# Kernel tuning notes

Hardware: AMD Instinct MI355X
Metric: run time of the kernel (lower is better)

## Reference

```python
import jax, jax.numpy as jnp
import numpy as np

D_MODEL = 96
D_EXP = 192      # d_expand == d_inner (ssm_ratio=ssm_rank_ratio=2)
D_STATE = 16
DT_RANK = 6      # ceil(96/16)
DC_IN = 4        # dc_inner
DC_STATE = 16
DTC_RANK = 6
B, H, W = 2, 48, 48


def _ln_channel(x, w, b):
    # WithBias LayerNorm over channel dim (torch code reshapes b c h w -> b (hw) c)
    mu = x.mean(axis=1, keepdims=True)
    var = ((x - mu) ** 2).mean(axis=1, keepdims=True)
    return (x - mu) / jnp.sqrt(var + 1e-5) * w[None, :, None, None] + b[None, :, None, None]


def _selective_scan(u, delta, A, Bs, Cs, D, delta_bias):
    # u, delta: (b,k,d,l); A: (k,d,n); Bs,Cs: (b,k,n,l); D, delta_bias: (k,d)
    delta = jax.nn.softplus(delta + delta_bias[None, :, :, None])
    dA = jnp.exp(jnp.einsum('bkdl,kdn->bkldn', delta, A))          # decay per step
    dBu = jnp.einsum('bkdl,bkdl,bknl->bkldn', delta, u, Bs)        # input injection

    def combine(c1, c2):
        a1, b1 = c1
        a2, b2 = c2
        return a1 * a2, a2 * b1 + b2

    _, hs = jax.lax.associative_scan(combine, (dA, dBu), axis=2)   # parallel linear recurrence over l
    return jnp.einsum('bkldn,bknl->bkdl', hs, Cs) + D[None, :, :, None] * u


def _spatial_core(x, x_proj_w, dt_w, dt_b, A_logs, Ds, onw, onb):
    b, d, h, w = x.shape
    l = h * w
    # cross_scan_2d: row-major, col-major, and their flips -> (b,4,d,l)
    xs = jnp.stack([x.reshape(b, d, l), jnp.swapaxes(x, 2, 3).reshape(b, d, l)], 1)
    xs = jnp.concatenate([xs, jnp.flip(xs, -1)], 1)
    x_dbl = jnp.einsum('bkdl,kcd->bkcl', xs, x_proj_w)
    dts, Bs, Cs = jnp.split(x_dbl, [DT_RANK, DT_RANK + D_STATE], axis=2)
    dts = jnp.einsum('bkrl,kdr->bkdl', dts, dt_w)
    A = -jnp.exp(A_logs).reshape(4, d, D_STATE)
    out_y = _selective_scan(xs, dts, A, Bs, Cs, Ds.reshape(4, d), dt_b)  # (b,4,d,l)
    inv = jnp.flip(out_y[:, 2:4], -1)
    wh = jnp.swapaxes(out_y[:, 1].reshape(b, d, w, h), 2, 3).reshape(b, d, l)
    invwh = jnp.swapaxes(inv[:, 1].reshape(b, d, w, h), 2, 3).reshape(b, d, l)
    y = (out_y[:, 0] + inv[:, 0] + wh + invwh).reshape(b, d, h, w)
    return _ln_channel(y, onw, onb)


def _channel_core(y, cin_w, cin_b, cout_w, cout_b, xc_proj_w, dtc_w, dtc_b, Ac_logs, Dsc, cnw, cnb):
    b, d = y.shape[0], y.shape[1]
    xc = y.mean(axis=(2, 3))                                              # adaptive avg pool -> (b,d)
    xc = xc[:, None, :] * cin_w.reshape(1, DC_IN, 1) + cin_b.reshape(1, DC_IN, 1)  # 1x1 conv_cin -> (b,4,d)
    xsc = jnp.stack([xc, jnp.flip(xc, -1)], 1)                            # (b,2,dc,L=d)
    xc_dbl = jnp.einsum('bkdl,kcd->bkcl', xsc, xc_proj_w)
    dtsc, Bc, Cc = jnp.split(xc_dbl, [DTC_RANK, DTC_RANK + DC_STATE], axis=2)
    dtsc = jnp.einsum('bkrl,kdr->bkdl', dtsc, dtc_w)
    Ac = -jnp.exp(Ac_logs).reshape(2, DC_IN, DC_STATE)
    outc = _selective_scan(xsc, dtsc, Ac, Bc, Cc, Dsc.reshape(2, DC_IN), dtc_b)  # (b,2,dc,d)
    yc = outc[:, 0] + jnp.flip(outc[:, 1], -1)                            # merge fwd/bwd channel scans
    yc = jnp.einsum('bdl,d->bl', yc, cout_w.reshape(DC_IN)) + cout_b.reshape(())  # 1x1 conv_cout
    return _ln_channel(yc.reshape(b, d, 1, 1), cnw, cnb)


def _conv1x1(x, w, b):
    return jnp.einsum('bchw,oc->bohw', x, w.reshape(w.shape[0], w.shape[1])) + b[None, :, None, None]


def _forward(x, in_w, in_b, dw_w, dw_b, x_proj_w, dt_w, dt_b, A_logs, Ds, out_norm_w, out_norm_b,
             cin_w, cin_b, cout_w, cout_b, xc_proj_w, dtc_w, dtc_b, Ac_logs, Dsc, cn_w, cn_b,
             out_w, out_b):
    xz = _conv1x1(x, in_w, in_b)                      # (b, 2*d_expand, h, w)
    x1, z = xz[:, :D_EXP], xz[:, D_EXP:]
    z = jax.nn.silu(z)
    x1 = jax.lax.conv_general_dilated(x1, dw_w, (1, 1), 'SAME',
                                      dimension_numbers=('NCHW', 'OIHW', 'NCHW'),
                                      feature_group_count=D_EXP) + dw_b[None, :, None, None]
    x1 = jax.nn.silu(x1)
    y = _spatial_core(x1, x_proj_w, dt_w, dt_b, A_logs, Ds, out_norm_w, out_norm_b)
    c = _channel_core(y, cin_w, cin_b, cout_w, cout_b, xc_proj_w, dtc_w, dtc_b, Ac_logs, Dsc, cn_w, cn_b)
    y = y * c * z                                     # channel modulation + gating
    return _conv1x1(y, out_w, out_b)


def setup_inputs():
    key = jax.random.key(0)
    ks = jax.random.split(key, 24)
    s = 0.02

    def rn(k, shape, scale=s):
        return jax.random.normal(k, shape, jnp.float32) * scale

    A_logs = jnp.log(jnp.tile(jnp.arange(1, D_STATE + 1, dtype=jnp.float32)[None, :], (4 * D_EXP, 1)))
    return dict(
        x=jax.random.normal(ks[0], (B, D_MODEL, H, W), jnp.float32),
        in_w=rn(ks[1], (2 * D_EXP, D_MODEL, 1, 1)),
        in_b=rn(ks[2], (2 * D_EXP,)),
        dw_w=rn(ks[3], (D_EXP, 1, 3, 3)),
        dw_b=rn(ks[4], (D_EXP,)),
        x_proj_w=rn(ks[5], (4, DT_RANK + 2 * D_STATE, D_EXP)),
        dt_w=rn(ks[6], (4, D_EXP, DT_RANK), 0.1),
        dt_b=rn(ks[7], (4, D_EXP), 0.5) - 4.0,
        A_logs=A_logs,
        Ds=jnp.ones((4 * D_EXP,), jnp.float32),
        out_norm_w=jnp.ones((D_EXP,), jnp.float32),
        out_norm_b=jnp.zeros((D_EXP,), jnp.float32),
        cin_w=rn(ks[8], (DC_IN, 1, 1, 1), 0.5),
        cin_b=rn(ks[9], (DC_IN,), 0.1),
        cout_w=rn(ks[10], (1, DC_IN, 1, 1), 0.5),
        cout_b=rn(ks[11], (1,), 0.1),
        xc_proj_w=rn(ks[12], (2, DTC_RANK + 2 * DC_STATE, DC_IN), 0.2),
        dtc_w=rn(ks[13], (2, DC_IN, DTC_RANK), 0.2),
        dtc_b=rn(ks[14], (2, DC_IN), 0.5),
        Ac_logs=rn(ks[15], (2 * DC_IN, DC_STATE), 1.0),
        Dsc=jnp.ones((2 * DC_IN,), jnp.float32),
        cn_w=jnp.ones((D_EXP,), jnp.float32),
        cn_b=jnp.zeros((D_EXP,), jnp.float32),
        out_w=rn(ks[16], (D_MODEL, D_EXP, 1, 1)),
        out_b=rn(ks[17], (D_MODEL,)),
    )


def reference(x, in_w, in_b, dw_w, dw_b, x_proj_w, dt_w, dt_b, A_logs, Ds, out_norm_w, out_norm_b,
              cin_w, cin_b, cout_w, cout_b, xc_proj_w, dtc_w, dtc_b, Ac_logs, Dsc, cn_w, cn_b,
              out_w, out_b):
    return _forward(x, in_w, in_b, dw_w, dw_b, x_proj_w, dt_w, dt_b, A_logs, Ds, out_norm_w, out_norm_b,
                    cin_w, cin_b, cout_w, cout_b, xc_proj_w, dtc_w, dtc_b, Ac_logs, Dsc, cn_w, cn_b,
                    out_w, out_b)
```

## Files before the change

### kernel.cpp

```cpp
#include <hip/hip_runtime.h>
#include <math.h>

#define DM 96
#define DE 192
#define LL 2304
#define NS 16
#define RK 6
#define NC 38
#define CH4 64
#define CL4 36

__device__ __forceinline__ float silu_f(float x){ return x / (1.f + __expf(-x)); }
__device__ __forceinline__ float softplus_f(float x){
  return (x > 20.f) ? x : __logf(1.f + __expf(x));
}

__device__ __forceinline__ int dir_map(int k, int l){
    switch(k){
      case 0: return l;
      case 1: return (l % 48) * 48 + l / 48;
      case 2: return 2303 - l;
      default: { int lr = 2303 - l; return (lr % 48) * 48 + lr / 48; }
    }
}

__global__ __launch_bounds__(384) void k1_conv_in(const float* __restrict__ x,
    const float* __restrict__ in_w, const float* __restrict__ in_b,
    float* __restrict__ x1raw, float* __restrict__ z){
  __shared__ float xv[DM*16];
  int tile = blockIdx.x;
  int b = tile / 144;
  int pos0 = (tile % 144) * 16;
  int tid = threadIdx.x;
  {
    int c = tid >> 2, p4 = tid & 3;
    float4 v = *(const float4*)(x + (b*DM + c)*LL + pos0 + p4*4);
    *(float4*)&xv[c*16 + p4*4] = v;
  }
  __syncthreads();
  float acc[16];
  #pragma unroll
  for (int p=0;p<16;p++) acc[p] = in_b[tid];
  const float4* wv4 = (const float4*)(in_w + tid*DM);
  #pragma unroll 4
  for (int c4=0;c4<24;c4++){
    float4 wv = wv4[c4];
    #pragma unroll
    for (int cc=0;cc<4;cc++){
      float w = (cc==0)?wv.x:((cc==1)?wv.y:((cc==2)?wv.z:wv.w));
      const float* xr = &xv[(c4*4+cc)*16];
      #pragma unroll
      for (int p4=0;p4<4;p4++){
        float4 xq = *(const float4*)&xr[p4*4];
        acc[p4*4+0] = fmaf(w, xq.x, acc[p4*4+0]);
        acc[p4*4+1] = fmaf(w, xq.y, acc[p4*4+1]);
        acc[p4*4+2] = fmaf(w, xq.z, acc[p4*4+2]);
        acc[p4*4+3] = fmaf(w, xq.w, acc[p4*4+3]);
      }
    }
  }
  if (tid < DE){
    float* dst = x1raw + (b*DE + tid)*LL + pos0;
    #pragma unroll
    for (int p4=0;p4<4;p4++)
      *(float4*)(dst + p4*4) = make_float4(acc[p4*4+0],acc[p4*4+1],acc[p4*4+2],acc[p4*4+3]);
  } else {
    int zc = tid - DE;
    float* dst = z + (b*DE + zc)*LL + pos0;
    #pragma unroll
    for (int p4=0;p4<4;p4++)
      *(float4*)(dst + p4*4) = make_float4(silu_f(acc[p4*4+0]),silu_f(acc[p4*4+1]),
                                           silu_f(acc[p4*4+2]),silu_f(acc[p4*4+3]));
  }
}

__global__ __launch_bounds__(256) void k2_dwconv(const float* __restrict__ x1raw,
    const float* __restrict__ dw_w, const float* __restrict__ dw_b,
    float* __restrict__ xconv, float* __restrict__ xconvT){
  __shared__ float lin[50][52];
  __shared__ float lout[48][50];
  int bd = blockIdx.x;
  int d = bd % DE;
  int tid = threadIdx.x;
  for (int i = tid; i < 50*52; i += 256) ((float*)lin)[i] = 0.f;
  __syncthreads();
  const float* src = x1raw + bd*LL;
  for (int i = tid; i < 576; i += 256){
    int r = i/12, c4 = (i%12)*4;
    float4 v = *(const float4*)(src + r*48 + c4);
    lin[r+1][c4+1] = v.x; lin[r+1][c4+2] = v.y; lin[r+1][c4+3] = v.z; lin[r+1][c4+4] = v.w;
  }
  float w00=dw_w[d*9+0], w01=dw_w[d*9+1], w02=dw_w[d*9+2];
  float w10=dw_w[d*9+3], w11=dw_w[d*9+4], w12=dw_w[d*9+5];
  float w20=dw_w[d*9+6], w21=dw_w[d*9+7], w22=dw_w[d*9+8];
  float bias = dw_b[d];
  __syncthreads();
  float* dst = xconv + bd*LL;
  for (int i = tid; i < 576; i += 256){
    int h = i/12, w4 = (i%12)*4;
    float o[4];
    #pragma unroll
    for (int j=0;j<4;j++){
      int w = w4 + j;
      float acc = bias;
      acc = fmaf(w00, lin[h  ][w], fmaf(w01, lin[h  ][w+1], fmaf(w02, lin[h  ][w+2], acc)));
      acc = fmaf(w10, lin[h+1][w], fmaf(w11, lin[h+1][w+1], fmaf(w12, lin[h+1][w+2], acc)));
      acc = fmaf(w20, lin[h+2][w], fmaf(w21, lin[h+2][w+1], fmaf(w22, lin[h+2][w+2], acc)));
      float v = silu_f(acc);
      o[j] = v;
      lout[h][w] = v;
    }
    *(float4*)(dst + h*48 + w4) = make_float4(o[0],o[1],o[2],o[3]);
  }
  __syncthreads();
  float* dstT = xconvT + bd*LL;
  for (int i = tid; i < 576; i += 256){
    int tw = i/12, th4 = (i%12)*4;
    float4 v = make_float4(lout[th4][tw], lout[th4+1][tw], lout[th4+2][tw], lout[th4+3][tw]);
    *(float4*)(dstT + tw*48 + th4) = v;
  }
}

__global__ __launch_bounds__(256) void k3_proj(const float* __restrict__ xconv,
    const float* __restrict__ xconvT,
    const float* __restrict__ x_proj_w, const float* __restrict__ dt_w,
    const float* __restrict__ dt_b, float* __restrict__ delta,
    float* __restrict__ Bs, float* __restrict__ Cs){
  __shared__ float smem[38*256];
  int bk = blockIdx.x / 36;
  int tile = blockIdx.x % 36;
  int b = bk >> 2, k = bk & 3;
  int tid = threadIdx.x;
  int lsub = tid & 63, dgrp = tid >> 6;
  int l = tile*64 + lsub;
  const float* wsrc = x_proj_w + k*NC*DE;
  for (int idx = tid; idx < NC*DE; idx += 256){
    int c = idx / DE, d = idx % DE;
    smem[d*40 + c] = wsrc[idx];
  }
  if (tid < DE){ smem[tid*40 + 38] = 0.f; smem[tid*40 + 39] = 0.f; }
  __syncthreads();
  float acc[40];
  #pragma unroll
  for (int c=0;c<40;c++) acc[c]=0.f;
  const float* uptr;
  {
    const float* basep = (k & 1) ? (xconvT + b*DE*LL) : (xconv + b*DE*LL);
    uptr = basep + ((k >= 2) ? (2303 - l) : l);
  }
  for (int dd=0; dd<48; dd++){
    int d = dgrp*48 + dd;
    float u = uptr[d*LL];
    const float4* wrow = (const float4*)&smem[d*40];
    #pragma unroll
    for (int j=0;j<10;j++){
      float4 wv = wrow[j];
      acc[j*4+0] = fmaf(u, wv.x, acc[j*4+0]);
      acc[j*4+1] = fmaf(u, wv.y, acc[j*4+1]);
      acc[j*4+2] = fmaf(u, wv.z, acc[j*4+2]);
      acc[j*4+3] = fmaf(u, wv.w, acc[j*4+3]);
    }
  }
  __syncthreads();
  #pragma unroll
  for (int c=0;c<38;c++) smem[c*256 + dgrp*64 + lsub] = acc[c];
  __syncthreads();
  for (int idx = tid; idx < 38*64; idx += 256){
    int c = idx >> 6, l2 = idx & 63;
    float s = smem[c*256 + l2] + smem[c*256 + 64 + l2]
            + smem[c*256 + 128 + l2] + smem[c*256 + 192 + l2];
    int lg = tile*64 + l2;
    if (c < RK){
      smem[c*256 + l2] = s;
    } else if (c < RK + NS){
      Bs[(bk*LL + lg)*NS + (c - RK)] = s;
    } else {
      Cs[(bk*LL + lg)*NS + (c - RK - NS)] = s;
    }
  }
  __syncthreads();
  float r0 = smem[0*256 + lsub], r1 = smem[1*256 + lsub], r2 = smem[2*256 + lsub];
  float r3 = smem[3*256 + lsub], r4 = smem[4*256 + lsub], r5 = smem[5*256 + lsub];
  const float* dwb = dt_w + k*DE*RK;
  const float* dbb = dt_b + k*DE;
  for (int dd=0; dd<48; dd++){
    int d = dgrp*48 + dd;
    const float* wr = dwb + d*RK;
    float t = dbb[d];
    t = fmaf(r0, wr[0], t); t = fmaf(r1, wr[1], t); t = fmaf(r2, wr[2], t);
    t = fmaf(r3, wr[3], t); t = fmaf(r4, wr[4], t); t = fmaf(r5, wr[5], t);
    delta[(bk*DE + d)*LL + l] = softplus_f(t);
  }
}

__global__ __launch_bounds__(1024) void k4_scan(const float* __restrict__ xconv,
    const float* __restrict__ xconvT,
    const float* __restrict__ delta, const float* __restrict__ Bs,
    const float* __restrict__ Cs, const float* __restrict__ A_logs,
    const float* __restrict__ Ds, float* __restrict__ ycomb){
  __shared__ float smem4[4*LL];
  float* sPf = smem4;
  float* sSf = smem4 + 4096;
  float* oyf = smem4;
  int gid = blockIdx.x;
  int b = gid / DE;
  int d = gid % DE;
  int tid = threadIdx.x;
  int k = tid >> 8;
  int sub = tid & 255;
  int c = sub >> 2, q = sub & 3;
  int bk = b*4 + k;
  const float LOG2E = 1.44269504f;
  float4 al = *(const float4*)&A_logs[(k*DE + d)*NS + q*4];
  float A2[4];
  A2[0] = -__expf(al.x)*LOG2E; A2[1] = -__expf(al.y)*LOG2E;
  A2[2] = -__expf(al.z)*LOG2E; A2[3] = -__expf(al.w)*LOG2E;
  float Dv = Ds[k*DE + d];
  const float* dptr = delta + (bk*DE + d)*LL;
  const float* ub = ((k & 1) ? xconvT : xconv) + (b*DE + d)*LL;
  bool rev = (k >= 2);
  const float* bbase = Bs + bk*LL*NS + q*4;
  const float* cbase = Cs + bk*LL*NS + q*4;
  int l0 = c*CL4;
  float sumdl = 0.f, S[4] = {0.f,0.f,0.f,0.f};
  #pragma unroll 3
  for (int i=0;i<CL4;i+=4){
    int l = l0 + i;
    float4 dl4 = *(const float4*)(dptr + l);
    float4 u4;
    if (!rev) u4 = *(const float4*)(ub + l);
    else { float4 t = *(const float4*)(ub + (LL-4) - l); u4 = make_float4(t.w,t.z,t.y,t.x); }
    #pragma unroll
    for (int j=0;j<4;j++){
      float dlj = (j==0)?dl4.x:((j==1)?dl4.y:((j==2)?dl4.z:dl4.w));
      float uj  = (j==0)?u4.x:((j==1)?u4.y:((j==2)?u4.z:u4.w));
      float du = dlj*uj;
      sumdl += dlj;
      float4 Bv = *(const float4*)(bbase + (l+j)*NS);
      float dA0 = exp2f(dlj*A2[0]); S[0] = fmaf(S[0], dA0, du*Bv.x);
      float dA1 = exp2f(dlj*A2[1]); S[1] = fmaf(S[1], dA1, du*Bv.y);
      float dA2 = exp2f(dlj*A2[2]); S[2] = fmaf(S[2], dA2, du*Bv.z);
      float dA3 = exp2f(dlj*A2[3]); S[3] = fmaf(S[3], dA3, du*Bv.w);
    }
  }
  *(float4*)&sPf[(k*CH4 + c)*NS + q*4] = make_float4(exp2f(A2[0]*sumdl), exp2f(A2[1]*sumdl),
                                                     exp2f(A2[2]*sumdl), exp2f(A2[3]*sumdl));
  *(float4*)&sSf[(k*CH4 + c)*NS + q*4] = make_float4(S[0],S[1],S[2],S[3]);
  __syncthreads();
  if (sub < NS){
    float hacc = 0.f;
    #pragma unroll 4
    for (int cc=0; cc<CH4; cc++){
      int idx = (k*CH4 + cc)*NS + sub;
      hacc = fmaf(hacc, sPf[idx], sSf[idx]);
      sSf[idx] = hacc;
    }
  }
  __syncthreads();
  float h[4];
  if (c == 0){ h[0]=h[1]=h[2]=h[3]=0.f; }
  else {
    float4 hi = *(const float4*)&sSf[(k*CH4 + c-1)*NS + q*4];
    h[0]=hi.x; h[1]=hi.y; h[2]=hi.z; h[3]=hi.w;
  }
  __syncthreads();
  #pragma unroll 3
  for (int i=0;i<CL4;i+=4){
    int l = l0 + i;
    float4 dl4 = *(const float4*)(dptr + l);
    float4 u4;
    if (!rev) u4 = *(const float4*)(ub + l);
    else { float4 t = *(const float4*)(ub + (LL-4) - l); u4 = make_float4(t.w,t.z,t.y,t.x); }
    #pragma unroll
    for (int j=0;j<4;j++){
      float dlj = (j==0)?dl4.x:((j==1)?dl4.y:((j==2)?dl4.z:dl4.w));
      float uj  = (j==0)?u4.x:((j==1)?u4.y:((j==2)?u4.z:u4.w));
      float du = dlj*uj;
      float4 Bv = *(const float4*)(bbase + (l+j)*NS);
      float4 Cv = *(const float4*)(cbase + (l+j)*NS);
      float dA0 = exp2f(dlj*A2[0]); h[0] = fmaf(h[0], dA0, du*Bv.x);
      float dA1 = exp2f(dlj*A2[1]); h[1] = fmaf(h[1], dA1, du*Bv.y);
      float dA2 = exp2f(dlj*A2[2]); h[2] = fmaf(h[2], dA2, du*Bv.z);
      float dA3 = exp2f(dlj*A2[3]); h[3] = fmaf(h[3], dA3, du*Bv.w);
      float py = h[0]*Cv.x + h[1]*Cv.y + h[2]*Cv.z + h[3]*Cv.w;
      py += __shfl_xor(py, 1);
      py += __shfl_xor(py, 2);
      if (q == 0){
        oyf[k*LL + dir_map(k, l+j)] = fmaf(Dv, uj, py);
      }
    }
  }
  __syncthreads();
  {
    float4* o4 = (float4*)(ycomb + (b*DE + d)*LL);
    const float4* s0 = (const float4*)(oyf);
    const float4* s1 = (const float4*)(oyf + LL);
    const float4* s2 = (const float4*)(oyf + 2*LL);
    const float4* s3 = (const float4*)(oyf + 3*LL);
    for (int i = tid; i < LL/4; i += 1024){
      float4 a = s0[i], e = s1[i], f = s2[i], g = s3[i];
      o4[i] = make_float4(a.x+e.x+f.x+g.x, a.y+e.y+f.y+g.y,
                          a.z+e.z+f.z+g.z, a.w+e.w+f.w+g.w);
    }
  }
}

__global__ __launch_bounds__(256) void k5_stats(const float* __restrict__ ycomb,
    float* __restrict__ mu_g, float* __restrict__ rs_g,
    float* __restrict__ partial){
  __shared__ float vals[DE][17];
  __shared__ float s_[16][16], s2_[16][16];
  __shared__ float mu_[16], rs_[16];
  int bT = blockIdx.x;
  int b = bT / 144;
  int pos0 = (bT % 144) * 16;
  int tid = threadIdx.x;
  int p = tid & 15, g = tid >> 4;
  const float* base = ycomb + b*DE*LL;
  float s = 0.f, s2 = 0.f;
  #pragma unroll
  for (int j=0;j<12;j++){
    int d = g*12 + j;
    float v = base[d*LL + pos0 + p];
    vals[d][p] = v;
    s += v; s2 += v*v;
  }
  s_[g][p] = s; s2_[g][p] = s2;
  __syncthreads();
  if (tid < 16){
    float ss = 0.f, ss2 = 0.f;
    #pragma unroll
    for (int gg=0; gg<16; gg++){ ss += s_[gg][tid]; ss2 += s2_[gg][tid]; }
    float mu = ss / DE;
    float var = ss2 / DE - mu*mu;
    mu_[tid] = mu; rs_[tid] = rsqrtf(var + 1e-5f);
    mu_g[b*LL + pos0 + tid] = mu;
    rs_g[b*LL + pos0 + tid] = rs_[tid];
  }
  __syncthreads();
  if (tid < DE){
    float ps = 0.f;
    #pragma unroll
    for (int pp=0;pp<16;pp++) ps += (vals[tid][pp] - mu_[pp]) * rs_[pp];
    partial[bT*DE + tid] = ps;
  }
}

__global__ __launch_bounds__(512) void k6b_channel(const float* __restrict__ partial,
    const float* __restrict__ onw, const float* __restrict__ onb,
    const float* __restrict__ cin_w, const float* __restrict__ cin_b,
    const float* __restrict__ cout_w, const float* __restrict__ cout_b,
    const float* __restrict__ xc_proj_w, const float* __restrict__ dtc_w,
    const float* __restrict__ dtc_b, const float* __restrict__ Ac_logs,
    const float* __restrict__ Dsc, const float* __restrict__ cn_w,
    const float* __restrict__ cn_b, float* __restrict__ cvec){
  __shared__ float xcs[DE];
  __shared__ float tmp[384];
  __shared__ float sP[128][4], sS[128][4];
  __shared__ float outc[2][4][DE];
  __shared__ float ycs[DE];
  __shared__ float muS, rsS;
  int b = blockIdx.x;
  int tid = threadIdx.x;
  if (tid < 384){
    int d = tid % DE, half = tid / DE;
    const float* pp = partial + (b*144 + half*72)*DE + d;
    float sacc = 0.f;
    #pragma unroll 8
    for (int t=0;t<72;t++) sacc += pp[t*DE];
    tmp[tid] = sacc;
  }
  __syncthreads();
  if (tid < DE) xcs[tid] = fmaf(onw[tid], (tmp[tid] + tmp[tid + DE]) * (1.f/LL), onb[tid]);
  __syncthreads();
  int chain = tid >> 2, ch = tid & 3;
  int k = chain >> 6, dc = (chain >> 4) & 3, n = chain & 15;
  const float LOG2E = 1.44269504f;
  float EW0=0,EW1=0,EW2=0,EW3=0;
  #pragma unroll
  for (int r=0;r<RK;r++){
    float dw = dtc_w[(k*4+dc)*RK + r];
    EW0 = fmaf(dw, xc_proj_w[(k*NC + r)*4 + 0], EW0);
    EW1 = fmaf(dw, xc_proj_w[(k*NC + r)*4 + 1], EW1);
    EW2 = fmaf(dw, xc_proj_w[(k*NC + r)*4 + 2], EW2);
    EW3 = fmaf(dw, xc_proj_w[(k*NC + r)*4 + 3], EW3);
  }
  float Bw0 = xc_proj_w[(k*NC + RK + n)*4 + 0];
  float Bw1 = xc_proj_w[(k*NC + RK + n)*4 + 1];
  float Bw2 = xc_proj_w[(k*NC + RK + n)*4 + 2];
  float Bw3 = xc_proj_w[(k*NC + RK + n)*4 + 3];
  float Cw0 = xc_proj_w[(k*NC + RK + NS + n)*4 + 0];
  float Cw1 = xc_proj_w[(k*NC + RK + NS + n)*4 + 1];
  float Cw2 = xc_proj_w[(k*NC + RK + NS + n)*4 + 2];
  float Cw3 = xc_proj_w[(k*NC + RK + NS + n)*4 + 3];
  float A2 = -__expf(Ac_logs[(k*4+dc)*NS + n]) * LOG2E;
  float Dv = Dsc[k*4+dc];
  float dtb = dtc_b[k*4+dc];
  float ciw0=cin_w[0], ciw1=cin_w[1], ciw2=cin_w[2], ciw3=cin_w[3];
  float cib0=cin_b[0], cib1=cin_b[1], cib2=cin_b[2], cib3=cin_b[3];
  int l0 = ch*48;
  float P = 1.f, S = 0.f;
  for (int i=0;i<48;i++){
    int lc = l0 + i;
    int lp = k ? (191 - lc) : lc;
    float xv = xcs[lp];
    float xs0 = fmaf(xv, ciw0, cib0);
    float xs1 = fmaf(xv, ciw1, cib1);
    float xs2 = fmaf(xv, ciw2, cib2);
    float xs3 = fmaf(xv, ciw3, cib3);
    float dt = dtb + xs0*EW0 + xs1*EW1 + xs2*EW2 + xs3*EW3;
    float dl = softplus_f(dt);
    float Bv = xs0*Bw0 + xs1*Bw1 + xs2*Bw2 + xs3*Bw3;
    float u = (dc==0)?xs0:((dc==1)?xs1:((dc==2)?xs2:xs3));
    float dA = exp2f(dl * A2);
    S = fmaf(S, dA, dl*u*Bv);
    P *= dA;
  }
  sP[chain][ch] = P; sS[chain][ch] = S;
  __syncthreads();
  if (tid < 128){
    float hacc = 0.f;
    #pragma unroll
    for (int cc=0; cc<4; cc++){
      hacc = fmaf(hacc, sP[tid][cc], sS[tid][cc]);
      sS[tid][cc] = hacc;
    }
  }
  __syncthreads();
  float h = (ch == 0) ? 0.f : sS[chain][ch-1];
  for (int i=0;i<48;i++){
    int lc = l0 + i;
    int lp = k ? (191 - lc) : lc;
    float xv = xcs[lp];
    float xs0 = fmaf(xv, ciw0, cib0);
    float xs1 = fmaf(xv, ciw1, cib1);
    float xs2 = fmaf(xv, ciw2, cib2);
    float xs3 = fmaf(xv, ciw3, cib3);
    float dt = dtb + xs0*EW0 + xs1*EW1 + xs2*EW2 + xs3*EW3;
    float dl = softplus_f(dt);
    float Bv = xs0*Bw0 + xs1*Bw1 + xs2*Bw2 + xs3*Bw3;
    float Cv = xs0*Cw0 + xs1*Cw1 + xs2*Cw2 + xs3*Cw3;
    float u = (dc==0)?xs0:((dc==1)?xs1:((dc==2)?xs2:xs3));
    float dA = exp2f(dl * A2);
    h = fmaf(h, dA, dl*u*Bv);
    float py = h * Cv;
    py += __shfl_xor(py, 4);
    py += __shfl_xor(py, 8);
    py += __shfl_xor(py, 16);
    py += __shfl_xor(py, 32);
    if (n == 0) outc[k][dc][lc] = fmaf(Dv, u, py);
  }
  __syncthreads();
  float co0=cout_w[0], co1=cout_w[1], co2=cout_w[2], co3=cout_w[3], cob=cout_b[0];
  for (int i = tid; i < DE; i += 512){
    float yv = cob
      + co0*(outc[0][0][i] + outc[1][0][191-i])
      + co1*(outc[0][1][i] + outc[1][1][191-i])
      + co2*(outc[0][2][i] + outc[1][2][191-i])
      + co3*(outc[0][3][i] + outc[1][3][191-i]);
    ycs[i] = yv;
  }
  __syncthreads();
  if (tid < 64){
    float s = 0.f, s2 = 0.f;
    #pragma unroll
    for (int j=0;j<3;j++){
      float v = ycs[tid + j*64];
      s += v; s2 += v*v;
    }
    for (int off=32; off>0; off>>=1){ s += __shfl_down(s, off); s2 += __shfl_down(s2, off); }
    if (tid == 0){
      float mu = s / DE;
      float var = s2 / DE - mu*mu;
      muS = mu; rsS = rsqrtf(var + 1e-5f);
    }
  }
  __syncthreads();
  float mu = muS, rs = rsS;
  for (int i = tid; i < DE; i += 512){
    cvec[b*DE + i] = (ycs[i] - mu) * rs * cn_w[i] + cn_b[i];
  }
}

__global__ __launch_bounds__(256) void k7_out(const float* __restrict__ ycomb,
    const float* __restrict__ mu_g, const float* __restrict__ rs_g,
    const float* __restrict__ onw, const float* __restrict__ onb,
    const float* __restrict__ cvec, const float* __restrict__ z,
    const float* __restrict__ out_w, const float* __restrict__ out_b,
    float* __restrict__ outp){
  __shared__ float t[DE*16];
  int tile = blockIdx.x;
  int b = tile / 144;
  int pos0 = (tile % 144) * 16;
  int tid = threadIdx.x;
  for (int i = tid; i < DE*4; i += 256){
    int c = i >> 2, p4 = (i & 3)*4;
    int gi = (b*DE + c)*LL + pos0 + p4;
    float4 yv = *(const float4*)(ycomb + gi);
    float4 zv = *(const float4*)(z + gi);
    float4 m4 = *(const float4*)(mu_g + b*LL + pos0 + p4);
    float4 r4 = *(const float4*)(rs_g + b*LL + pos0 + p4);
    float w = onw[c], bb = onb[c];
    float cv = cvec[b*DE + c];
    float t0 = fmaf((yv.x - m4.x)*r4.x, w, bb) * cv * zv.x;
    float t1 = fmaf((yv.y - m4.y)*r4.y, w, bb) * cv * zv.y;
    float t2 = fmaf((yv.z - m4.z)*r4.z, w, bb) * cv * zv.z;
    float t3 = fmaf((yv.w - m4.w)*r4.w, w, bb) * cv * zv.w;
    *(float4*)&t[c*16 + p4] = make_float4(t0,t1,t2,t3);
  }
  __syncthreads();
  for (int j = tid; j < DM*16; j += 256){
    int o = j >> 4, p = j & 15;
    float acc = out_b[o];
    const float4* wr4 = (const float4*)(out_w + o*DE);
    #pragma unroll 8
    for (int c4=0;c4<48;c4++){
      float4 wv = wr4[c4];
      acc = fmaf(wv.x, t[(c4*4+0)*16+p], acc);
      acc = fmaf(wv.y, t[(c4*4+1)*16+p], acc);
      acc = fmaf(wv.z, t[(c4*4+2)*16+p], acc);
      acc = fmaf(wv.w, t[(c4*4+3)*16+p], acc);
    }
    outp[(b*DM + o)*LL + pos0 + p] = acc;
  }
}

extern "C" void kernel_launch(void* const* d_in, const int* in_sizes, int n_in,
                              void* d_out, int out_size, void* d_ws, size_t ws_size,
                              hipStream_t stream){
  const float* x        = (const float*)d_in[0];
  const float* in_w     = (const float*)d_in[1];
  const float* in_b     = (const float*)d_in[2];
  const float* dw_w     = (const float*)d_in[3];
  const float* dw_b     = (const float*)d_in[4];
  const float* x_proj_w = (const float*)d_in[5];
  const float* dt_w     = (const float*)d_in[6];
  const float* dt_b     = (const float*)d_in[7];
  const float* A_logs   = (const float*)d_in[8];
  const float* Ds       = (const float*)d_in[9];
  const float* onw      = (const float*)d_in[10];
  const float* onb      = (const float*)d_in[11];
  const float* cin_w    = (const float*)d_in[12];
  const float* cin_b    = (const float*)d_in[13];
  const float* cout_w   = (const float*)d_in[14];
  const float* cout_b   = (const float*)d_in[15];
  const float* xc_proj_w= (const float*)d_in[16];
  const float* dtc_w    = (const float*)d_in[17];
  const float* dtc_b    = (const float*)d_in[18];
  const float* Ac_logs  = (const float*)d_in[19];
  const float* Dsc      = (const float*)d_in[20];
  const float* cn_w     = (const float*)d_in[21];
  const float* cn_b     = (const float*)d_in[22];
  const float* out_w    = (const float*)d_in[23];
  const float* out_b    = (const float*)d_in[24];

  float* ws = (float*)d_ws;
  float* x1raw = ws;  ws += 2*DE*LL;
  float* zbuf  = ws;  ws += 2*DE*LL;
  float* xconv = ws;  ws += 2*DE*LL;
  float* xconvT= ws;  ws += 2*DE*LL;
  float* delta = ws;  ws += 2*4*DE*LL;
  float* Bsb   = ws;  ws += 2*4*LL*NS;
  float* Csb   = ws;  ws += 2*4*LL*NS;
  float* ycomb = ws;  ws += 2*DE*LL;
  float* cvec  = ws;  ws += 2*DE;
  float* partial = ws; ws += 2*144*DE;
  float* mu_g  = ws;  ws += 2*LL;
  float* rs_g  = ws;  ws += 2*LL;

  hipLaunchKernelGGL(k1_conv_in, dim3(288), dim3(384), 0, stream, x, in_w, in_b, x1raw, zbuf);
  hipLaunchKernelGGL(k2_dwconv, dim3(384), dim3(256), 0, stream, x1raw, dw_w, dw_b, xconv, xconvT);
  hipLaunchKernelGGL(k3_proj, dim3(288), dim3(256), 0, stream, xconv, xconvT, x_proj_w, dt_w, dt_b, delta, Bsb, Csb);
  hipLaunchKernelGGL(k4_scan, dim3(384), dim3(1024), 0, stream, xconv, xconvT, delta, Bsb, Csb, A_logs, Ds, ycomb);
  hipLaunchKernelGGL(k5_stats, dim3(288), dim3(256), 0, stream, ycomb, mu_g, rs_g, partial);
  hipLaunchKernelGGL(k6b_channel, dim3(2), dim3(512), 0, stream, partial, onw, onb, cin_w, cin_b, cout_w, cout_b,
                     xc_proj_w, dtc_w, dtc_b, Ac_logs, Dsc, cn_w, cn_b, cvec);
  hipLaunchKernelGGL(k7_out, dim3(288), dim3(256), 0, stream, ycomb, mu_g, rs_g, onw, onb, cvec, zbuf, out_w, out_b, (float*)d_out);
}
```

Baseline: 192.6 us.

## Interleave scan inputs by chunk and split scan blocks per direction

k3_proj now writes delta, B and C in a chunk-interleaved layout (position l stored at (l%36)*64 + l/36). This lets the 64 chunk threads of k4_scan read consecutive addresses on each step, so their loads coalesce. k4_scan runs one 256-thread block per (batch, direction, channel) instead of one 1024-thread block covering all four directions, and stages the input row in shared memory. The four direction outputs now go to a new out_y buffer of four times the size, and k5 sums them and writes ycomb. This adds extra global write and read traffic in exchange for better occupancy and coalescing in the scan.

```diff
diff --git a/kernel.cpp b/kernel.cpp
--- a/kernel.cpp
+++ b/kernel.cpp
@@ -124,8 +124,8 @@
 __global__ __launch_bounds__(256) void k3_proj(const float* __restrict__ xconv,
     const float* __restrict__ xconvT,
     const float* __restrict__ x_proj_w, const float* __restrict__ dt_w,
-    const float* __restrict__ dt_b, float* __restrict__ delta,
-    float* __restrict__ Bs, float* __restrict__ Cs){
+    const float* __restrict__ dt_b, float* __restrict__ delta2,
+    float* __restrict__ B2, float* __restrict__ C2){
   __shared__ float smem[38*256];
   int bk = blockIdx.x / 36;
   int tile = blockIdx.x % 36;
@@ -170,12 +170,13 @@
     float s = smem[c*256 + l2] + smem[c*256 + 64 + l2]
             + smem[c*256 + 128 + l2] + smem[c*256 + 192 + l2];
     int lg = tile*64 + l2;
+    int so = (lg % 36)*64 + (lg / 36);
     if (c < RK){
       smem[c*256 + l2] = s;
     } else if (c < RK + NS){
-      Bs[(bk*LL + lg)*NS + (c - RK)] = s;
+      B2[bk*36864 + so*16 + (c - RK)] = s;
     } else {
-      Cs[(bk*LL + lg)*NS + (c - RK - NS)] = s;
+      C2[bk*36864 + so*16 + (c - RK - NS)] = s;
     }
   }
   __syncthreads();
@@ -183,130 +184,111 @@
   float r3 = smem[3*256 + lsub], r4 = smem[4*256 + lsub], r5 = smem[5*256 + lsub];
   const float* dwb = dt_w + k*DE*RK;
   const float* dbb = dt_b + k*DE;
+  int so_l = (l % 36)*64 + (l / 36);
   for (int dd=0; dd<48; dd++){
     int d = dgrp*48 + dd;
     const float* wr = dwb + d*RK;
     float t = dbb[d];
     t = fmaf(r0, wr[0], t); t = fmaf(r1, wr[1], t); t = fmaf(r2, wr[2], t);
     t = fmaf(r3, wr[3], t); t = fmaf(r4, wr[4], t); t = fmaf(r5, wr[5], t);
-    delta[(bk*DE + d)*LL + l] = softplus_f(t);
-  }
-}
-
-__global__ __launch_bounds__(1024) void k4_scan(const float* __restrict__ xconv,
+    delta2[(bk*DE + d)*LL + so_l] = softplus_f(t);
+  }
+}
+
+__global__ __launch_bounds__(256, 6) void k4_scan(const float* __restrict__ xconv,
     const float* __restrict__ xconvT,
-    const float* __restrict__ delta, const float* __restrict__ Bs,
-    const float* __restrict__ Cs, const float* __restrict__ A_logs,
-    const float* __restrict__ Ds, float* __restrict__ ycomb){
-  __shared__ float smem4[4*LL];
-  float* sPf = smem4;
-  float* sSf = smem4 + 4096;
-  float* oyf = smem4;
+    const float* __restrict__ delta2, const float* __restrict__ B2,
+    const float* __restrict__ C2, const float* __restrict__ A_logs,
+    const float* __restrict__ Ds, float* __restrict__ out_y){
+  __shared__ float smem[2*LL];
+  float* us  = smem;
+  float* sPf = smem + LL;
+  float* sSf = smem + LL + 1024;
+  float* oyf = smem + LL;
   int gid = blockIdx.x;
-  int b = gid / DE;
-  int d = gid % DE;
-  int tid = threadIdx.x;
-  int k = tid >> 8;
-  int sub = tid & 255;
-  int c = sub >> 2, q = sub & 3;
+  int b = gid / (4*DE);
+  int kd = gid % (4*DE);
+  int k = kd / DE;
+  int d = kd % DE;
   int bk = b*4 + k;
+  int tid = threadIdx.x;
+  int c = tid >> 2, q = tid & 3;
   const float LOG2E = 1.44269504f;
   float4 al = *(const float4*)&A_logs[(k*DE + d)*NS + q*4];
   float A2[4];
   A2[0] = -__expf(al.x)*LOG2E; A2[1] = -__expf(al.y)*LOG2E;
   A2[2] = -__expf(al.z)*LOG2E; A2[3] = -__expf(al.w)*LOG2E;
   float Dv = Ds[k*DE + d];
-  const float* dptr = delta + (bk*DE + d)*LL;
-  const float* ub = ((k & 1) ? xconvT : xconv) + (b*DE + d)*LL;
+  {
+    const float4* ub4 = (const float4*)(((k & 1) ? xconvT : xconv) + (b*DE + d)*LL);
+    float4* us4 = (float4*)us;
+    for (int j = tid; j < LL/4; j += 256) us4[j] = ub4[j];
+  }
+  const float* dbase = delta2 + (bk*DE + d)*LL;
+  const float* bbase = B2 + bk*36864 + q*4;
+  const float* cbase = C2 + bk*36864 + q*4;
   bool rev = (k >= 2);
-  const float* bbase = Bs + bk*LL*NS + q*4;
-  const float* cbase = Cs + bk*LL*NS + q*4;
   int l0 = c*CL4;
+  __syncthreads();
   float sumdl = 0.f, S[4] = {0.f,0.f,0.f,0.f};
-  #pragma unroll 3
-  for (int i=0;i<CL4;i+=4){
-    int l = l0 + i;
-    float4 dl4 = *(const float4*)(dptr + l);
-    float4 u4;
-    if (!rev) u4 = *(const float4*)(ub + l);
-    else { float4 t = *(const float4*)(ub + (LL-4) - l); u4 = make_float4(t.w,t.z,t.y,t.x); }
-    #pragma unroll
-    for (int j=0;j<4;j++){
-      float dlj = (j==0)?dl4.x:((j==1)?dl4.y:((j==2)?dl4.z:dl4.w));
-      float uj  = (j==0)?u4.x:((j==1)?u4.y:((j==2)?u4.z:u4.w));
-      float du = dlj*uj;
-      sumdl += dlj;
-      float4 Bv = *(const float4*)(bbase + (l+j)*NS);
-      float dA0 = exp2f(dlj*A2[0]); S[0] = fmaf(S[0], dA0, du*Bv.x);
-      float dA1 = exp2f(dlj*A2[1]); S[1] = fmaf(S[1], dA1, du*Bv.y);
-      float dA2 = exp2f(dlj*A2[2]); S[2] = fmaf(S[2], dA2, du*Bv.z);
-      float dA3 = exp2f(dlj*A2[3]); S[3] = fmaf(S[3], dA3, du*Bv.w);
-    }
-  }
-  *(float4*)&sPf[(k*CH4 + c)*NS + q*4] = make_float4(exp2f(A2[0]*sumdl), exp2f(A2[1]*sumdl),
-                                                     exp2f(A2[2]*sumdl), exp2f(A2[3]*sumdl));
-  *(float4*)&sSf[(k*CH4 + c)*NS + q*4] = make_float4(S[0],S[1],S[2],S[3]);
-  __syncthreads();
-  if (sub < NS){
+  #pragma unroll 4
+  for (int i=0;i<CL4;i++){
+    float dl = dbase[i*64 + c];
+    float u  = us[rev ? (2303 - (l0+i)) : (l0+i)];
+    float du = dl*u;
+    sumdl += dl;
+    float4 Bv = *(const float4*)(bbase + (i*64 + c)*16);
+    float dA0 = exp2f(dl*A2[0]); S[0] = fmaf(S[0], dA0, du*Bv.x);
+    float dA1 = exp2f(dl*A2[1]); S[1] = fmaf(S[1], dA1, du*Bv.y);
+    float dA2 = exp2f(dl*A2[2]); S[2] = fmaf(S[2], dA2, du*Bv.z);
+    float dA3 = exp2f(dl*A2[3]); S[3] = fmaf(S[3], dA3, du*Bv.w);
+  }
+  *(float4*)&sPf[c*NS + q*4] = make_float4(exp2f(A2[0]*sumdl), exp2f(A2[1]*sumdl),
+                                           exp2f(A2[2]*sumdl), exp2f(A2[3]*sumdl));
+  *(float4*)&sSf[c*NS + q*4] = make_float4(S[0],S[1],S[2],S[3]);
+  __syncthreads();
+  if (tid < NS){
     float hacc = 0.f;
     #pragma unroll 4
     for (int cc=0; cc<CH4; cc++){
-      int idx = (k*CH4 + cc)*NS + sub;
-      hacc = fmaf(hacc, sPf[idx], sSf[idx]);
-      sSf[idx] = hacc;
+      hacc = fmaf(hacc, sPf[cc*NS + tid], sSf[cc*NS + tid]);
+      sSf[cc*NS + tid] = hacc;
     }
   }
   __syncthreads();
   float h[4];
   if (c == 0){ h[0]=h[1]=h[2]=h[3]=0.f; }
-  else {
-    float4 hi = *(const float4*)&sSf[(k*CH4 + c-1)*NS + q*4];
-    h[0]=hi.x; h[1]=hi.y; h[2]=hi.z; h[3]=hi.w;
-  }
-  __syncthreads();
-  #pragma unroll 3
-  for (int i=0;i<CL4;i+=4){
+  else { float4 hi = *(const float4*)&sSf[(c-1)*NS + q*4]; h[0]=hi.x; h[1]=hi.y; h[2]=hi.z; h[3]=hi.w; }
+  __syncthreads();
+  #pragma unroll 2
+  for (int i=0;i<CL4;i++){
     int l = l0 + i;
-    float4 dl4 = *(const float4*)(dptr + l);
-    float4 u4;
-    if (!rev) u4 = *(const float4*)(ub + l);
-    else { float4 t = *(const float4*)(ub + (LL-4) - l); u4 = make_float4(t.w,t.z,t.y,t.x); }
-    #pragma unroll
-    for (int j=0;j<4;j++){
-      float dlj = (j==0)?dl4.x:((j==1)?dl4.y:((j==2)?dl4.z:dl4.w));
-      float uj  = (j==0)?u4.x:((j==1)?u4.y:((j==2)?u4.z:u4.w));
-      float du = dlj*uj;
-      float4 Bv = *(const float4*)(bbase + (l+j)*NS);
-      float4 Cv = *(const float4*)(cbase + (l+j)*NS);
-      float dA0 = exp2f(dlj*A2[0]); h[0] = fmaf(h[0], dA0, du*Bv.x);
-      float dA1 = exp2f(dlj*A2[1]); h[1] = fmaf(h[1], dA1, du*Bv.y);
-      float dA2 = exp2f(dlj*A2[2]); h[2] = fmaf(h[2], dA2, du*Bv.z);
-      float dA3 = exp2f(dlj*A2[3]); h[3] = fmaf(h[3], dA3, du*Bv.w);
-      float py = h[0]*Cv.x + h[1]*Cv.y + h[2]*Cv.z + h[3]*Cv.w;
-      py += __shfl_xor(py, 1);
-      py += __shfl_xor(py, 2);
-      if (q == 0){
-        oyf[k*LL + dir_map(k, l+j)] = fmaf(Dv, uj, py);
-      }
+    float dl = dbase[i*64 + c];
+    float u  = us[rev ? (2303 - l) : l];
+    float du = dl*u;
+    float4 Bv = *(const float4*)(bbase + (i*64 + c)*16);
+    float4 Cv = *(const float4*)(cbase + (i*64 + c)*16);
+    float dA0 = exp2f(dl*A2[0]); h[0] = fmaf(h[0], dA0, du*Bv.x);
+    float dA1 = exp2f(dl*A2[1]); h[1] = fmaf(h[1], dA1, du*Bv.y);
+    float dA2 = exp2f(dl*A2[2]); h[2] = fmaf(h[2], dA2, du*Bv.z);
+    float dA3 = exp2f(dl*A2[3]); h[3] = fmaf(h[3], dA3, du*Bv.w);
+    float py = h[0]*Cv.x + h[1]*Cv.y + h[2]*Cv.z + h[3]*Cv.w;
+    py += __shfl_xor(py, 1);
+    py += __shfl_xor(py, 2);
+    if (q == 0){
+      oyf[dir_map(k, l)] = fmaf(Dv, u, py);
     }
   }
   __syncthreads();
   {
-    float4* o4 = (float4*)(ycomb + (b*DE + d)*LL);
-    const float4* s0 = (const float4*)(oyf);
-    const float4* s1 = (const float4*)(oyf + LL);
-    const float4* s2 = (const float4*)(oyf + 2*LL);
-    const float4* s3 = (const float4*)(oyf + 3*LL);
-    for (int i = tid; i < LL/4; i += 1024){
-      float4 a = s0[i], e = s1[i], f = s2[i], g = s3[i];
-      o4[i] = make_float4(a.x+e.x+f.x+g.x, a.y+e.y+f.y+g.y,
-                          a.z+e.z+f.z+g.z, a.w+e.w+f.w+g.w);
-    }
-  }
-}
-
-__global__ __launch_bounds__(256) void k5_stats(const float* __restrict__ ycomb,
-    float* __restrict__ mu_g, float* __restrict__ rs_g,
+    float4* o4 = (float4*)(out_y + (bk*DE + d)*LL);
+    const float4* s4 = (const float4*)oyf;
+    for (int i = tid; i < LL/4; i += 256) o4[i] = s4[i];
+  }
+}
+
+__global__ __launch_bounds__(256) void k5_combine(const float* __restrict__ out_y,
+    float* __restrict__ ycomb, float* __restrict__ mu_g, float* __restrict__ rs_g,
     float* __restrict__ partial){
   __shared__ float vals[DE][17];
   __shared__ float s_[16][16], s2_[16][16];
@@ -316,12 +298,13 @@
   int pos0 = (bT % 144) * 16;
   int tid = threadIdx.x;
   int p = tid & 15, g = tid >> 4;
-  const float* base = ycomb + b*DE*LL;
+  const float* base = out_y + b*4*DE*LL;
   float s = 0.f, s2 = 0.f;
   #pragma unroll
   for (int j=0;j<12;j++){
     int d = g*12 + j;
-    float v = base[d*LL + pos0 + p];
+    int idx = d*LL + pos0 + p;
+    float v = base[idx] + base[DE*LL + idx] + base[2*DE*LL + idx] + base[3*DE*LL + idx];
     vals[d][p] = v;
     s += v; s2 += v*v;
   }
@@ -336,6 +319,13 @@
     mu_[tid] = mu; rs_[tid] = rsqrtf(var + 1e-5f);
     mu_g[b*LL + pos0 + tid] = mu;
     rs_g[b*LL + pos0 + tid] = rs_[tid];
+  }
+  __syncthreads();
+  float mu = mu_[p], rs = rs_[p];
+  #pragma unroll
+  for (int j=0;j<12;j++){
+    int d = g*12 + j;
+    ycomb[(b*DE + d)*LL + pos0 + p] = vals[d][p];
   }
   __syncthreads();
   if (tid < DE){
@@ -559,9 +549,10 @@
   float* zbuf  = ws;  ws += 2*DE*LL;
   float* xconv = ws;  ws += 2*DE*LL;
   float* xconvT= ws;  ws += 2*DE*LL;
-  float* delta = ws;  ws += 2*4*DE*LL;
-  float* Bsb   = ws;  ws += 2*4*LL*NS;
-  float* Csb   = ws;  ws += 2*4*LL*NS;
+  float* delta2= ws;  ws += 2*4*DE*LL;
+  float* B2    = ws;  ws += 2*4*LL*NS;
+  float* C2    = ws;  ws += 2*4*LL*NS;
+  float* outy  = ws;  ws += 2*4*DE*LL;
   float* ycomb = ws;  ws += 2*DE*LL;
   float* cvec  = ws;  ws += 2*DE;
   float* partial = ws; ws += 2*144*DE;
@@ -570,9 +561,9 @@
 
   hipLaunchKernelGGL(k1_conv_in, dim3(288), dim3(384), 0, stream, x, in_w, in_b, x1raw, zbuf);
   hipLaunchKernelGGL(k2_dwconv, dim3(384), dim3(256), 0, stream, x1raw, dw_w, dw_b, xconv, xconvT);
-  hipLaunchKernelGGL(k3_proj, dim3(288), dim3(256), 0, stream, xconv, xconvT, x_proj_w, dt_w, dt_b, delta, Bsb, Csb);
-  hipLaunchKernelGGL(k4_scan, dim3(384), dim3(1024), 0, stream, xconv, xconvT, delta, Bsb, Csb, A_logs, Ds, ycomb);
-  hipLaunchKernelGGL(k5_stats, dim3(288), dim3(256), 0, stream, ycomb, mu_g, rs_g, partial);
+  hipLaunchKernelGGL(k3_proj, dim3(288), dim3(256), 0, stream, xconv, xconvT, x_proj_w, dt_w, dt_b, delta2, B2, C2);
+  hipLaunchKernelGGL(k4_scan, dim3(1536), dim3(256), 0, stream, xconv, xconvT, delta2, B2, C2, A_logs, Ds, outy);
+  hipLaunchKernelGGL(k5_combine, dim3(288), dim3(256), 0, stream, outy, ycomb, mu_g, rs_g, partial);
   hipLaunchKernelGGL(k6b_channel, dim3(2), dim3(512), 0, stream, partial, onw, onb, cin_w, cin_b, cout_w, cout_b,
                      xc_proj_w, dtc_w, dtc_b, Ac_logs, Dsc, cn_w, cn_b, cvec);
   hipLaunchKernelGGL(k7_out, dim3(288), dim3(256), 0, stream, ycomb, mu_g, rs_g, onw, onb, cvec, zbuf, out_w, out_b, (float*)d_out);
```

New measurement: 199.2 us. 3.4% more time.
